# Kernel tuning notes

Hardware: AMD Instinct MI355X
Metric: run time of the kernel (lower is better)

## Reference

```python
import jax, jax.numpy as jnp
import numpy as np

EMBED = 128
HEADS = 8
HEAD_DIM = EMBED // HEADS

def setup_inputs() -> dict:
    key = jax.random.key(0)
    ks = jax.random.split(key, 8)
    B, N = 2, 4096
    values = jax.random.normal(ks[0], (B, N, EMBED), dtype=jnp.float32)
    keys = jax.random.normal(ks[1], (B, N, EMBED), dtype=jnp.float32)
    query = jax.random.normal(ks[2], (B, N, EMBED), dtype=jnp.float32)
    s = 1.0 / np.sqrt(HEAD_DIM)
    Wv = jax.random.normal(ks[3], (HEAD_DIM, HEAD_DIM), dtype=jnp.float32) * s
    Wk = jax.random.normal(ks[4], (HEAD_DIM, HEAD_DIM), dtype=jnp.float32) * s
    Wq = jax.random.normal(ks[5], (HEAD_DIM, HEAD_DIM), dtype=jnp.float32) * s
    Wo = jax.random.normal(ks[6], (EMBED, EMBED), dtype=jnp.float32) * (1.0 / np.sqrt(EMBED))
    bo = jnp.zeros((EMBED,), dtype=jnp.float32)
    return {"values": values, "keys": keys, "query": query,
            "Wv": Wv, "Wk": Wk, "Wq": Wq, "Wo": Wo, "bo": bo}

def reference(values, keys, query, Wv, Wk, Wq, Wo, bo):
    B, N, _ = query.shape
    # split heads: [B,N,H,Dh]
    v = values.reshape(B, N, HEADS, HEAD_DIM)
    k = keys.reshape(B, N, HEADS, HEAD_DIM)
    q = query.reshape(B, N, HEADS, HEAD_DIM)
    # per-head linear (torch Linear: x @ W.T), same weight for all heads
    v = jnp.einsum('bnhd,ed->bnhe', v, Wv)
    k = jnp.einsum('bnhd,ed->bnhe', k, Wk)
    q = jnp.einsum('bnhd,ed->bnhe', q, Wq)
    # scores [B,H,N,N], note scale by sqrt(embed_size) as in original
    energy = jnp.einsum('bqhd,bkhd->bhqk', q, k) / jnp.sqrt(jnp.float32(EMBED))
    attn = jax.nn.softmax(energy, axis=-1)
    out = jnp.einsum('bhql,blhd->bqhd', attn, v).reshape(B, N, EMBED)
    return out @ Wo.T + bo
```

## Files before the change

kernel.cpp:

```cpp
#include <hip/hip_runtime.h>

#define BB 2
#define NN 4096
#define HH 8
#define DD 16
#define EE 128
#define LBLK 128
#define NSPL 4
#define NTH (NN / NSPL / LBLK)

typedef _Float16 f16;
typedef _Float16 f16x4 __attribute__((ext_vector_type(4)));
typedef _Float16 f16x2 __attribute__((ext_vector_type(2)));
typedef _Float16 f16x8 __attribute__((ext_vector_type(8)));
typedef __fp16 h16x2 __attribute__((ext_vector_type(2)));
typedef float f32x4 __attribute__((ext_vector_type(4)));

#define QSCALE 0.12751741f

__global__ __launch_bounds__(256) void proj_kernel(
    const float* __restrict__ vals, const float* __restrict__ keys,
    const float* __restrict__ query,
    const float* __restrict__ Wv, const float* __restrict__ Wk,
    const float* __restrict__ Wq, const float* __restrict__ Wo,
    f16* __restrict__ Qp, f16* __restrict__ Kp, f16* __restrict__ Vt,
    f16* __restrict__ Wo16)
{
    if (blockIdx.x >= 768) {
        const int i = (blockIdx.x - 768) * 256 + threadIdx.x;
        Wo16[i] = (f16)Wo[i];
        return;
    }
    __shared__ float W[256];
    const int p = blockIdx.x >> 8;
    const float* Wsrc = (p == 0) ? Wv : ((p == 1) ? Wk : Wq);
    W[threadIdx.x] = Wsrc[threadIdx.x];
    __syncthreads();

    const int idx = ((blockIdx.x & 255) << 8) | threadIdx.x;
    const int n = idx & 4095;
    const int h = (idx >> 12) & 7;
    const int b = idx >> 15;

    const float* xsrc = (p == 0) ? vals : ((p == 1) ? keys : query);
    const float4* xp = (const float4*)(xsrc + (size_t)(b * NN + n) * EE + h * DD);
    const float4 x0 = xp[0], x1 = xp[1], x2 = xp[2], x3 = xp[3];
    const float scale = (p == 2) ? QSCALE : 1.0f;

    alignas(16) f16 out[16];
    #pragma unroll
    for (int e = 0; e < 16; e++) {
        const float4* wr = (const float4*)(W + e * 16);
        const float4 w0 = wr[0], w1 = wr[1], w2 = wr[2], w3 = wr[3];
        float acc = x0.x * w0.x + x0.y * w0.y + x0.z * w0.z + x0.w * w0.w
                  + x1.x * w1.x + x1.y * w1.y + x1.z * w1.z + x1.w * w1.w
                  + x2.x * w2.x + x2.y * w2.y + x2.z * w2.z + x2.w * w2.w
                  + x3.x * w3.x + x3.y * w3.y + x3.z * w3.z + x3.w * w3.w;
        out[e] = (f16)(acc * scale);
    }

    if (p == 0) {
        f16* dst = Vt + (size_t)(b * HH + h) * DD * NN + n;
        #pragma unroll
        for (int e = 0; e < 16; e++) dst[(size_t)e * NN] = out[e];
    } else {
        f16* dst = ((p == 1) ? Kp : Qp) + (size_t)((b * HH + h) * NN + n) * DD;
        ((uint4*)dst)[0] = ((const uint4*)out)[0];
        ((uint4*)dst)[1] = ((const uint4*)out)[1];
    }
}

__global__ __launch_bounds__(256, 8) void attn_kernel(
    const f16* __restrict__ Qp, const f16* __restrict__ Kp,
    const f16* __restrict__ Vt, float* __restrict__ Oacc,
    float* __restrict__ den)
{
    __shared__ alignas(16) f16 Kl[2][2048];
    __shared__ alignas(16) f16 Vl[2][2048];

    const int tid = threadIdx.x;
    const int lane = tid & 63;
    const int wave = tid >> 6;
    const int r = lane & 15;
    const int g = lane >> 4;

    const int bid = blockIdx.x;
    const int quarter = bid & 3;
    const int qt = (bid >> 2) & 31;
    const int bh = bid >> 7;
    const int q0 = qt * 128 + wave * 32;
    const int L0 = quarter * (NN / NSPL);

    const bool isK = tid < 128;
    const f16* gbase;
    int w0, w1;
    size_t gstep;
    if (isK) {
        const int spair = tid >> 6;
        const int lp = tid & 63;
        const int rr = lp & 15, gg = lp >> 4;
        const int lam = 8 * (rr >> 2) + (rr & 3);
        gbase = Kp + ((size_t)bh * NN + L0 + 64 * spair + lam) * DD + 4 * gg;
        gstep = (size_t)LBLK * DD;
        w0 = (2 * spair) * 512 + lp * 8;
        w1 = (2 * spair + 1) * 512 + lp * 8;
    } else {
        const int v = tid - 128;
        gbase = Vt + ((size_t)bh * DD + (v & 15)) * NN + L0 + 32 * (v >> 6) + 8 * ((v >> 4) & 3);
        gstep = (size_t)LBLK;
        w0 = v * 8;
        w1 = 1024 + v * 8;
    }

    const f16x4 qf0 = *(const f16x4*)(Qp + ((size_t)bh * NN + q0 + r) * DD + 4 * g);
    const f16x4 qf1 = *(const f16x4*)(Qp + ((size_t)bh * NN + q0 + 16 + r) * DD + 4 * g);

    f16x8 sA, sB;
#define STAGE_LOAD() { \
    if (isK) { \
        const f16x4 a0 = *(const f16x4*)(gbase + 0); \
        const f16x4 a1 = *(const f16x4*)(gbase + 64); \
        const f16x4 a2 = *(const f16x4*)(gbase + 512); \
        const f16x4 a3 = *(const f16x4*)(gbase + 576); \
        sA = __builtin_shufflevector(a0, a1, 0,1,2,3,4,5,6,7); \
        sB = __builtin_shufflevector(a2, a3, 0,1,2,3,4,5,6,7); \
    } else { \
        sA = *(const f16x8*)(gbase + 0); \
        sB = *(const f16x8*)(gbase + 64); \
    } \
    gbase += gstep; }

    STAGE_LOAD();
    {
        f16* wp = isK ? &Kl[0][0] : &Vl[0][0];
        *(f16x8*)(wp + w0) = sA;
        *(f16x8*)(wp + w1) = sB;
    }
    __syncthreads();

    f32x4 acc0 = {0.f,0.f,0.f,0.f}, acc1 = {0.f,0.f,0.f,0.f};
    float da0 = 0.f, db0 = 0.f, da1 = 0.f, db1 = 0.f;
    const h16x2 ones = {(__fp16)1.0f, (__fp16)1.0f};
    int cur = 0;

#define PROCESS(QF, ACC, DA, DB) { \
    const f32x4 z = {0.f,0.f,0.f,0.f}; \
    const f32x4 st0 = __builtin_amdgcn_mfma_f32_16x16x16f16(kfA, (QF), z, 0, 0, 0); \
    const f32x4 st1 = __builtin_amdgcn_mfma_f32_16x16x16f16(kfB, (QF), z, 0, 0, 0); \
    const float e0 = __builtin_amdgcn_exp2f(st0[0]); \
    const float e1 = __builtin_amdgcn_exp2f(st0[1]); \
    const float e2 = __builtin_amdgcn_exp2f(st0[2]); \
    const float e3 = __builtin_amdgcn_exp2f(st0[3]); \
    const float f0 = __builtin_amdgcn_exp2f(st1[0]); \
    const float f1 = __builtin_amdgcn_exp2f(st1[1]); \
    const float f2 = __builtin_amdgcn_exp2f(st1[2]); \
    const float f3 = __builtin_amdgcn_exp2f(st1[3]); \
    const h16x2 h0 = __builtin_amdgcn_cvt_pkrtz(e0, e1); \
    const h16x2 h1 = __builtin_amdgcn_cvt_pkrtz(e2, e3); \
    const h16x2 h2 = __builtin_amdgcn_cvt_pkrtz(f0, f1); \
    const h16x2 h3 = __builtin_amdgcn_cvt_pkrtz(f2, f3); \
    DA = __builtin_amdgcn_fdot2(h0, ones, DA, false); \
    DA = __builtin_amdgcn_fdot2(h1, ones, DA, false); \
    DB = __builtin_amdgcn_fdot2(h2, ones, DB, false); \
    DB = __builtin_amdgcn_fdot2(h3, ones, DB, false); \
    const f16x4 pA = __builtin_shufflevector( \
        __builtin_bit_cast(f16x2, h0), __builtin_bit_cast(f16x2, h1), 0, 1, 2, 3); \
    const f16x4 pB = __builtin_shufflevector( \
        __builtin_bit_cast(f16x2, h2), __builtin_bit_cast(f16x2, h3), 0, 1, 2, 3); \
    const f16x8 pf8 = __builtin_shufflevector(pA, pB, 0, 1, 2, 3, 4, 5, 6, 7); \
    ACC = __builtin_amdgcn_mfma_f32_16x16x32_f16(vf8, pf8, ACC, 0, 0, 0); }

    for (int t = 0; t < NTH; ++t) {
        if (t < NTH - 1) STAGE_LOAD();

        const f16* Kb = &Kl[cur][0];
        const f16* Vb = &Vl[cur][0];
        #pragma unroll
        for (int s = 0; s < 4; ++s) {
            const f16x8 kf8 = *(const f16x8*)(Kb + s * 512 + lane * 8);
            const f16x8 vf8 = *(const f16x8*)(Vb + s * 512 + lane * 8);
            const f16x4 kfA = __builtin_shufflevector(kf8, kf8, 0, 1, 2, 3);
            const f16x4 kfB = __builtin_shufflevector(kf8, kf8, 4, 5, 6, 7);
            PROCESS(qf0, acc0, da0, db0)
            PROCESS(qf1, acc1, da1, db1)
        }

        if (t < NTH - 1) {
            f16* wp = (isK ? &Kl[cur ^ 1][0] : &Vl[cur ^ 1][0]);
            *(f16x8*)(wp + w0) = sA;
            *(f16x8*)(wp + w1) = sB;
        }
        __syncthreads();
        cur ^= 1;
    }
#undef PROCESS
#undef STAGE_LOAD

    float d0 = da0 + db0;
    d0 += __shfl_xor(d0, 16, 64);
    d0 += __shfl_xor(d0, 32, 64);
    float d1 = da1 + db1;
    d1 += __shfl_xor(d1, 16, 64);
    d1 += __shfl_xor(d1, 32, 64);

    const int b = bh >> 3, h = bh & 7;
    float* OaccQ = Oacc + (size_t)quarter * (BB * NN * EE);
    *(f32x4*)(OaccQ + ((size_t)(b * NN + q0 + r)) * EE + h * DD + 4 * g) = acc0;
    *(f32x4*)(OaccQ + ((size_t)(b * NN + q0 + 16 + r)) * EE + h * DD + 4 * g) = acc1;
    if (lane < 16) {
        den[(size_t)(quarter * 16 + bh) * NN + q0 + lane] = d0;
        den[(size_t)(quarter * 16 + bh) * NN + q0 + 16 + lane] = d1;
    }
}

__global__ __launch_bounds__(256) void outproj_kernel(
    const float* __restrict__ Oacc, const float* __restrict__ den,
    const f16* __restrict__ Wo16, const float* __restrict__ bo,
    float* __restrict__ out)
{
    const int lane = threadIdx.x & 63;
    const int wave = threadIdx.x >> 6;
    const int r = lane & 15;
    const int g = lane >> 4;
    const int n0 = (blockIdx.x * 2 + (wave >> 1)) * 16;
    const int eh = (wave & 1) * 4;

    const int n = n0 + r;
    const int b = n >> 12;
    const int nn = n & 4095;
    const float* Oa0 = Oacc + (size_t)n * EE;
    const float* Oa1 = Oa0 + (size_t)1 * (BB * NN * EE);
    const float* Oa2 = Oa0 + (size_t)2 * (BB * NN * EE);
    const float* Oa3 = Oa0 + (size_t)3 * (BB * NN * EE);

    f32x4 acc[4];
    #pragma unroll
    for (int e = 0; e < 4; e++) acc[e] = (f32x4){0.f, 0.f, 0.f, 0.f};

    #pragma unroll
    for (int k0 = 0; k0 < 8; k0++) {
        const size_t didx = (size_t)(b * 8 + k0) * NN + nn;
        const float inv = 1.0f / ((den[didx] + den[(size_t)16 * NN + didx])
                                + (den[(size_t)32 * NN + didx] + den[(size_t)48 * NN + didx]));
        const f32x4 xa = *(const f32x4*)(Oa0 + k0 * 16 + 4 * g)
                       + *(const f32x4*)(Oa1 + k0 * 16 + 4 * g)
                       + *(const f32x4*)(Oa2 + k0 * 16 + 4 * g)
                       + *(const f32x4*)(Oa3 + k0 * 16 + 4 * g);
        const float s0 = xa[0] * inv;
        const float s1 = xa[1] * inv;
        const float s2 = xa[2] * inv;
        const float s3 = xa[3] * inv;
        const f16x4 a = __builtin_shufflevector(
            __builtin_bit_cast(f16x2, __builtin_amdgcn_cvt_pkrtz(s0, s1)),
            __builtin_bit_cast(f16x2, __builtin_amdgcn_cvt_pkrtz(s2, s3)), 0, 1, 2, 3);
        #pragma unroll
        for (int e = 0; e < 4; e++) {
            const f16x4 bf = *(const f16x4*)(Wo16 + (size_t)((eh + e) * 16 + r) * EE + k0 * 16 + 4 * g);
            acc[e] = __builtin_amdgcn_mfma_f32_16x16x16f16(a, bf, acc[e], 0, 0, 0);
        }
    }

    #pragma unroll
    for (int e = 0; e < 4; e++) {
        const float bias = bo[(eh + e) * 16 + r];
        #pragma unroll
        for (int i = 0; i < 4; i++) {
            out[(size_t)(n0 + 4 * g + i) * EE + (eh + e) * 16 + r] = acc[e][i] + bias;
        }
    }
}

extern "C" void kernel_launch(void* const* d_in, const int* in_sizes, int n_in,
                              void* d_out, int out_size, void* d_ws, size_t ws_size,
                              hipStream_t stream)
{
    const float* vals  = (const float*)d_in[0];
    const float* keys  = (const float*)d_in[1];
    const float* query = (const float*)d_in[2];
    const float* Wv    = (const float*)d_in[3];
    const float* Wk    = (const float*)d_in[4];
    const float* Wq    = (const float*)d_in[5];
    const float* Wo    = (const float*)d_in[6];
    const float* bo    = (const float*)d_in[7];
    float* out = (float*)d_out;

    char* w = (char*)d_ws;
    f16*   Qp   = (f16*)(w);
    f16*   Kp   = (f16*)(w + (2u << 20));
    f16*   Vt   = (f16*)(w + (4u << 20));
    f16*   Wo16 = (f16*)(w + (6u << 20));
    float* den  = (float*)(w + (6u << 20) + 65536);
    float* Oacc = (float*)(w + (8u << 20));

    hipLaunchKernelGGL(proj_kernel, dim3(832), dim3(256), 0, stream,
                       vals, keys, query, Wv, Wk, Wq, Wo, Qp, Kp, Vt, Wo16);
    hipLaunchKernelGGL(attn_kernel, dim3(2048), dim3(256), 0, stream,
                       Qp, Kp, Vt, Oacc, den);
    hipLaunchKernelGGL(outproj_kernel, dim3(256), dim3(256), 0, stream,
                       Oacc, den, Wo16, bo, out);
}
```

Measured before the change: 58.47 us.

## Load K and V fragments directly from global memory, dropping LDS staging

The attention kernel no longer stages K and V tiles through double-buffered shared memory with a barrier per tile. Each wave now loads its own MFMA fragments straight from global memory, relying on L1/L2 caching since all four waves in a block read the same K/V data. This removes the LDS writes and reads and the __syncthreads calls. In exchange it adds redundant global traffic per block and exposes global load latency, with no explicit prefetch.

```diff
diff --git a/kernel.cpp b/kernel.cpp
--- a/kernel.cpp
+++ b/kernel.cpp
@@ -75,9 +75,6 @@
     const f16* __restrict__ Vt, float* __restrict__ Oacc,
     float* __restrict__ den)
 {
-    __shared__ alignas(16) f16 Kl[2][2048];
-    __shared__ alignas(16) f16 Vl[2][2048];
-
     const int tid = threadIdx.x;
     const int lane = tid & 63;
     const int wave = tid >> 6;
@@ -91,57 +88,16 @@
     const int q0 = qt * 128 + wave * 32;
     const int L0 = quarter * (NN / NSPL);
 
-    const bool isK = tid < 128;
-    const f16* gbase;
-    int w0, w1;
-    size_t gstep;
-    if (isK) {
-        const int spair = tid >> 6;
-        const int lp = tid & 63;
-        const int rr = lp & 15, gg = lp >> 4;
-        const int lam = 8 * (rr >> 2) + (rr & 3);
-        gbase = Kp + ((size_t)bh * NN + L0 + 64 * spair + lam) * DD + 4 * gg;
-        gstep = (size_t)LBLK * DD;
-        w0 = (2 * spair) * 512 + lp * 8;
-        w1 = (2 * spair + 1) * 512 + lp * 8;
-    } else {
-        const int v = tid - 128;
-        gbase = Vt + ((size_t)bh * DD + (v & 15)) * NN + L0 + 32 * (v >> 6) + 8 * ((v >> 4) & 3);
-        gstep = (size_t)LBLK;
-        w0 = v * 8;
-        w1 = 1024 + v * 8;
-    }
+    const int lam = 8 * (r >> 2) + (r & 3);
+    const f16* kptr = Kp + ((size_t)bh * NN + L0 + lam) * DD + 4 * g;
+    const f16* vptr = Vt + ((size_t)bh * DD + r) * NN + L0 + 8 * g;
 
     const f16x4 qf0 = *(const f16x4*)(Qp + ((size_t)bh * NN + q0 + r) * DD + 4 * g);
     const f16x4 qf1 = *(const f16x4*)(Qp + ((size_t)bh * NN + q0 + 16 + r) * DD + 4 * g);
-
-    f16x8 sA, sB;
-#define STAGE_LOAD() { \
-    if (isK) { \
-        const f16x4 a0 = *(const f16x4*)(gbase + 0); \
-        const f16x4 a1 = *(const f16x4*)(gbase + 64); \
-        const f16x4 a2 = *(const f16x4*)(gbase + 512); \
-        const f16x4 a3 = *(const f16x4*)(gbase + 576); \
-        sA = __builtin_shufflevector(a0, a1, 0,1,2,3,4,5,6,7); \
-        sB = __builtin_shufflevector(a2, a3, 0,1,2,3,4,5,6,7); \
-    } else { \
-        sA = *(const f16x8*)(gbase + 0); \
-        sB = *(const f16x8*)(gbase + 64); \
-    } \
-    gbase += gstep; }
-
-    STAGE_LOAD();
-    {
-        f16* wp = isK ? &Kl[0][0] : &Vl[0][0];
-        *(f16x8*)(wp + w0) = sA;
-        *(f16x8*)(wp + w1) = sB;
-    }
-    __syncthreads();
 
     f32x4 acc0 = {0.f,0.f,0.f,0.f}, acc1 = {0.f,0.f,0.f,0.f};
     float da0 = 0.f, db0 = 0.f, da1 = 0.f, db1 = 0.f;
     const h16x2 ones = {(__fp16)1.0f, (__fp16)1.0f};
-    int cur = 0;
 
 #define PROCESS(QF, ACC, DA, DB) { \
     const f32x4 z = {0.f,0.f,0.f,0.f}; \
@@ -171,30 +127,18 @@
     ACC = __builtin_amdgcn_mfma_f32_16x16x32_f16(vf8, pf8, ACC, 0, 0, 0); }
 
     for (int t = 0; t < NTH; ++t) {
-        if (t < NTH - 1) STAGE_LOAD();
-
-        const f16* Kb = &Kl[cur][0];
-        const f16* Vb = &Vl[cur][0];
         #pragma unroll
         for (int s = 0; s < 4; ++s) {
-            const f16x8 kf8 = *(const f16x8*)(Kb + s * 512 + lane * 8);
-            const f16x8 vf8 = *(const f16x8*)(Vb + s * 512 + lane * 8);
-            const f16x4 kfA = __builtin_shufflevector(kf8, kf8, 0, 1, 2, 3);
-            const f16x4 kfB = __builtin_shufflevector(kf8, kf8, 4, 5, 6, 7);
+            const f16x4 kfA = *(const f16x4*)(kptr + (size_t)(32 * s) * DD);
+            const f16x4 kfB = *(const f16x4*)(kptr + (size_t)(32 * s + 4) * DD);
+            const f16x8 vf8 = *(const f16x8*)(vptr + 32 * s);
             PROCESS(qf0, acc0, da0, db0)
             PROCESS(qf1, acc1, da1, db1)
         }
-
-        if (t < NTH - 1) {
-            f16* wp = (isK ? &Kl[cur ^ 1][0] : &Vl[cur ^ 1][0]);
-            *(f16x8*)(wp + w0) = sA;
-            *(f16x8*)(wp + w1) = sB;
-        }
-        __syncthreads();
-        cur ^= 1;
+        kptr += (size_t)LBLK * DD;
+        vptr += (size_t)LBLK;
     }
 #undef PROCESS
-#undef STAGE_LOAD
 
     float d0 = da0 + db0;
     d0 += __shfl_xor(d0, 16, 64);
```

After: 73.15 us. 1.25x slower.

## Double attention block size and compute softmax denominator with MFMA

Applied to the files above, without the earlier changes.

The attention kernel now uses 512-thread blocks covering 256 queries. Each iteration stages two 128-key tiles into shared memory, which halves the number of blocks and of barrier rounds per key range. The row-sum denominator is now taken from an extra MFMA against a ones matrix instead of fdot2 plus cross-lane shuffles. This trades extra matrix-core work and larger LDS use per block for fewer VALU ops and syncs, and it may lower occupancy.

```diff
diff --git a/kernel.cpp b/kernel.cpp
--- a/kernel.cpp
+++ b/kernel.cpp
@@ -7,7 +7,7 @@
 #define EE 128
 #define LBLK 128
 #define NSPL 4
-#define NTH (NN / NSPL / LBLK)
+#define NIV 4
 
 typedef _Float16 f16;
 typedef _Float16 f16x4 __attribute__((ext_vector_type(4)));
@@ -70,13 +70,13 @@
     }
 }
 
-__global__ __launch_bounds__(256, 8) void attn_kernel(
+__global__ __launch_bounds__(512, 8) void attn_kernel(
     const f16* __restrict__ Qp, const f16* __restrict__ Kp,
     const f16* __restrict__ Vt, float* __restrict__ Oacc,
     float* __restrict__ den)
 {
-    __shared__ alignas(16) f16 Kl[2][2048];
-    __shared__ alignas(16) f16 Vl[2][2048];
+    __shared__ alignas(16) f16 Kl[2][2][2048];
+    __shared__ alignas(16) f16 Vl[2][2][2048];
 
     const int tid = threadIdx.x;
     const int lane = tid & 63;
@@ -86,31 +86,32 @@
 
     const int bid = blockIdx.x;
     const int quarter = bid & 3;
-    const int qt = (bid >> 2) & 31;
-    const int bh = bid >> 7;
-    const int q0 = qt * 128 + wave * 32;
+    const int qt = (bid >> 2) & 15;
+    const int bh = bid >> 6;
+    const int q0 = qt * 256 + wave * 32;
     const int L0 = quarter * (NN / NSPL);
 
-    const bool isK = tid < 128;
+    const int ti = tid >> 8;
+    const int u = tid & 255;
+    const bool isK = u < 128;
     const f16* gbase;
     int w0, w1;
-    size_t gstep;
     if (isK) {
-        const int spair = tid >> 6;
-        const int lp = tid & 63;
+        const int spair = u >> 6;
+        const int lp = u & 63;
         const int rr = lp & 15, gg = lp >> 4;
         const int lam = 8 * (rr >> 2) + (rr & 3);
-        gbase = Kp + ((size_t)bh * NN + L0 + 64 * spair + lam) * DD + 4 * gg;
-        gstep = (size_t)LBLK * DD;
+        gbase = Kp + ((size_t)bh * NN + L0 + ti * LBLK + 64 * spair + lam) * DD + 4 * gg;
         w0 = (2 * spair) * 512 + lp * 8;
         w1 = (2 * spair + 1) * 512 + lp * 8;
     } else {
-        const int v = tid - 128;
-        gbase = Vt + ((size_t)bh * DD + (v & 15)) * NN + L0 + 32 * (v >> 6) + 8 * ((v >> 4) & 3);
-        gstep = (size_t)LBLK;
+        const int v = u - 128;
+        gbase = Vt + ((size_t)bh * DD + (v & 15)) * NN + L0 + ti * LBLK
+                   + 32 * (v >> 6) + 8 * ((v >> 4) & 3);
         w0 = v * 8;
         w1 = 1024 + v * 8;
     }
+    const size_t gstep = isK ? (size_t)(2 * LBLK) * DD : (size_t)(2 * LBLK);
 
     const f16x4 qf0 = *(const f16x4*)(Qp + ((size_t)bh * NN + q0 + r) * DD + 4 * g);
     const f16x4 qf1 = *(const f16x4*)(Qp + ((size_t)bh * NN + q0 + 16 + r) * DD + 4 * g);
@@ -130,23 +131,24 @@
     } \
     gbase += gstep; }
 
+#define STAGE_WRITE(HALF) { \
+    f16* wp = isK ? &Kl[HALF][ti][0] : &Vl[HALF][ti][0]; \
+    *(f16x8*)(wp + w0) = sA; \
+    *(f16x8*)(wp + w1) = sB; }
+
     STAGE_LOAD();
-    {
-        f16* wp = isK ? &Kl[0][0] : &Vl[0][0];
-        *(f16x8*)(wp + w0) = sA;
-        *(f16x8*)(wp + w1) = sB;
-    }
+    STAGE_WRITE(0);
     __syncthreads();
 
     f32x4 acc0 = {0.f,0.f,0.f,0.f}, acc1 = {0.f,0.f,0.f,0.f};
-    float da0 = 0.f, db0 = 0.f, da1 = 0.f, db1 = 0.f;
-    const h16x2 ones = {(__fp16)1.0f, (__fp16)1.0f};
-    int cur = 0;
-
-#define PROCESS(QF, ACC, DA, DB) { \
-    const f32x4 z = {0.f,0.f,0.f,0.f}; \
-    const f32x4 st0 = __builtin_amdgcn_mfma_f32_16x16x16f16(kfA, (QF), z, 0, 0, 0); \
-    const f32x4 st1 = __builtin_amdgcn_mfma_f32_16x16x16f16(kfB, (QF), z, 0, 0, 0); \
+    f32x4 dacc0 = {0.f,0.f,0.f,0.f}, dacc1 = {0.f,0.f,0.f,0.f};
+    const f32x4 zz = {0.f,0.f,0.f,0.f};
+    const f16x8 ones8 = {(f16)1.f,(f16)1.f,(f16)1.f,(f16)1.f,
+                         (f16)1.f,(f16)1.f,(f16)1.f,(f16)1.f};
+
+#define QKPV(QF, ACC, DACC) { \
+    const f32x4 st0 = __builtin_amdgcn_mfma_f32_16x16x16f16(kfA, (QF), zz, 0, 0, 0); \
+    const f32x4 st1 = __builtin_amdgcn_mfma_f32_16x16x16f16(kfB, (QF), zz, 0, 0, 0); \
     const float e0 = __builtin_amdgcn_exp2f(st0[0]); \
     const float e1 = __builtin_amdgcn_exp2f(st0[1]); \
     const float e2 = __builtin_amdgcn_exp2f(st0[2]); \
@@ -159,57 +161,48 @@
     const h16x2 h1 = __builtin_amdgcn_cvt_pkrtz(e2, e3); \
     const h16x2 h2 = __builtin_amdgcn_cvt_pkrtz(f0, f1); \
     const h16x2 h3 = __builtin_amdgcn_cvt_pkrtz(f2, f3); \
-    DA = __builtin_amdgcn_fdot2(h0, ones, DA, false); \
-    DA = __builtin_amdgcn_fdot2(h1, ones, DA, false); \
-    DB = __builtin_amdgcn_fdot2(h2, ones, DB, false); \
-    DB = __builtin_amdgcn_fdot2(h3, ones, DB, false); \
     const f16x4 pA = __builtin_shufflevector( \
         __builtin_bit_cast(f16x2, h0), __builtin_bit_cast(f16x2, h1), 0, 1, 2, 3); \
     const f16x4 pB = __builtin_shufflevector( \
         __builtin_bit_cast(f16x2, h2), __builtin_bit_cast(f16x2, h3), 0, 1, 2, 3); \
     const f16x8 pf8 = __builtin_shufflevector(pA, pB, 0, 1, 2, 3, 4, 5, 6, 7); \
-    ACC = __builtin_amdgcn_mfma_f32_16x16x32_f16(vf8, pf8, ACC, 0, 0, 0); }
-
-    for (int t = 0; t < NTH; ++t) {
-        if (t < NTH - 1) STAGE_LOAD();
-
-        const f16* Kb = &Kl[cur][0];
-        const f16* Vb = &Vl[cur][0];
-        #pragma unroll
-        for (int s = 0; s < 4; ++s) {
-            const f16x8 kf8 = *(const f16x8*)(Kb + s * 512 + lane * 8);
-            const f16x8 vf8 = *(const f16x8*)(Vb + s * 512 + lane * 8);
-            const f16x4 kfA = __builtin_shufflevector(kf8, kf8, 0, 1, 2, 3);
-            const f16x4 kfB = __builtin_shufflevector(kf8, kf8, 4, 5, 6, 7);
-            PROCESS(qf0, acc0, da0, db0)
-            PROCESS(qf1, acc1, da1, db1)
+    ACC  = __builtin_amdgcn_mfma_f32_16x16x32_f16(vf8, pf8, ACC, 0, 0, 0); \
+    DACC = __builtin_amdgcn_mfma_f32_16x16x32_f16(ones8, pf8, DACC, 0, 0, 0); }
+
+    int half = 0;
+    for (int iv = 0; iv < NIV; ++iv) {
+        if (iv < NIV - 1) STAGE_LOAD();
+
+        #pragma unroll
+        for (int t2 = 0; t2 < 2; ++t2) {
+            const f16* Kb = &Kl[half][t2][0];
+            const f16* Vb = &Vl[half][t2][0];
+            #pragma unroll
+            for (int s = 0; s < 4; ++s) {
+                const f16x8 kf8 = *(const f16x8*)(Kb + s * 512 + lane * 8);
+                const f16x8 vf8 = *(const f16x8*)(Vb + s * 512 + lane * 8);
+                const f16x4 kfA = __builtin_shufflevector(kf8, kf8, 0, 1, 2, 3);
+                const f16x4 kfB = __builtin_shufflevector(kf8, kf8, 4, 5, 6, 7);
+                QKPV(qf0, acc0, dacc0)
+                QKPV(qf1, acc1, dacc1)
+            }
         }
 
-        if (t < NTH - 1) {
-            f16* wp = (isK ? &Kl[cur ^ 1][0] : &Vl[cur ^ 1][0]);
-            *(f16x8*)(wp + w0) = sA;
-            *(f16x8*)(wp + w1) = sB;
-        }
+        if (iv < NIV - 1) STAGE_WRITE(half ^ 1);
         __syncthreads();
-        cur ^= 1;
-    }
-#undef PROCESS
+        half ^= 1;
+    }
+#undef QKPV
+#undef STAGE_WRITE
 #undef STAGE_LOAD
-
-    float d0 = da0 + db0;
-    d0 += __shfl_xor(d0, 16, 64);
-    d0 += __shfl_xor(d0, 32, 64);
-    float d1 = da1 + db1;
-    d1 += __shfl_xor(d1, 16, 64);
-    d1 += __shfl_xor(d1, 32, 64);
 
     const int b = bh >> 3, h = bh & 7;
     float* OaccQ = Oacc + (size_t)quarter * (BB * NN * EE);
     *(f32x4*)(OaccQ + ((size_t)(b * NN + q0 + r)) * EE + h * DD + 4 * g) = acc0;
     *(f32x4*)(OaccQ + ((size_t)(b * NN + q0 + 16 + r)) * EE + h * DD + 4 * g) = acc1;
     if (lane < 16) {
-        den[(size_t)(quarter * 16 + bh) * NN + q0 + lane] = d0;
-        den[(size_t)(quarter * 16 + bh) * NN + q0 + 16 + lane] = d1;
+        den[(size_t)(quarter * 16 + bh) * NN + q0 + lane] = dacc0[0];
+        den[(size_t)(quarter * 16 + bh) * NN + q0 + 16 + lane] = dacc1[0];
     }
 }
 
@@ -294,7 +287,7 @@
 
     hipLaunchKernelGGL(proj_kernel, dim3(832), dim3(256), 0, stream,
                        vals, keys, query, Wv, Wk, Wq, Wo, Qp, Kp, Vt, Wo16);
-    hipLaunchKernelGGL(attn_kernel, dim3(2048), dim3(256), 0, stream,
+    hipLaunchKernelGGL(attn_kernel, dim3(1024), dim3(512), 0, stream,
                        Qp, Kp, Vt, Oacc, den);
     hipLaunchKernelGGL(outproj_kernel, dim3(256), dim3(256), 0, stream,
                        Oacc, den, Wo16, bo, out);
```

Result: faster. 54.33 us (-7.1%).
